# Optimization experiments

Hardware: AMD Instinct MI355X
Metric: run time of the kernel (lower is better)

## Reference

```python
import jax, jax.numpy as jnp
import numpy as np
from jax import lax

N_VAR, BATCH, N_IN, N_OUT, N_FEAT, T = 4, 32, 32, 32, 32, 256
EPS, COUPLING, GMAX, GMIN = 0.05, 0.2, 10.0, 0.01
DT, RMIN, RMAX, CMIN, CMAX = 0.1, 1e5, 1e7, 1e-7, 1e-4
ETA = np.array([0.05, 0.5, 0.3, 3.0], dtype=np.float32)  # printed-tanh activation params


def _init_theta(key, n_in, n_out):
    # xavier_uniform -> min-max normalize to [0,1], then bias-column construction as in pLayer.__init__
    a = float(np.sqrt(6.0 / (n_in + 2 + n_out)))
    t = jax.random.uniform(key, (n_in + 2, n_out), minval=-a, maxval=a)
    t = (t - t.min()) / (t.max() - t.min())
    t = t.at[-1, :].add(GMAX)
    t = t.at[-2, :].set(ETA[2] / (1.0 - ETA[2]) * (t[:-2].sum(0) + t[-1]))
    return t.astype(jnp.float32)


def setup_inputs():
    key = jax.random.key(0)
    kx, k1, k2 = jax.random.split(key, 3)
    x = jax.random.uniform(kx, (N_VAR, BATCH, N_IN, T), dtype=jnp.float32)
    theta1_ = _init_theta(k1, N_IN, N_OUT)
    theta2_ = _init_theta(k2, N_OUT * (N_FEAT + 1), N_OUT)
    # LearnableFilter init from beta_init (C_ fixed at -10, R_ is logit of normalized R)
    betas = np.linspace(0.1, 0.9, N_OUT)
    b0 = betas[:N_FEAT]
    b1 = betas[::-1][:N_FEAT]
    C_mean = 1.0 / (1.0 + np.exp(10.0)) * (CMAX - CMIN) + CMIN
    def r_(b):
        R_true = b * DT / (1.0 - b) / C_mean
        Rn = (R_true - RMIN) / (RMAX - RMIN)
        return np.log(Rn / (1.0 - Rn))
    Rlf_ = jnp.asarray(np.broadcast_to(np.stack([r_(b0), r_(b1)], -1), (N_OUT, N_FEAT, 2)).copy(), dtype=jnp.float32)
    Clf_ = jnp.full((N_OUT, N_FEAT, 2), -10.0, dtype=jnp.float32)
    return {"x": x, "theta1_": theta1_, "theta2_": theta2_, "Rlf_": Rlf_, "Clf_": Clf_}


def _theta_eff(theta_):
    # clamp + magnitude pruning with straight-through estimator
    t = jnp.clip(theta_, -GMAX, GMAX)
    t = jnp.where(jnp.abs(t) < GMIN, 0.0, t)
    return lax.stop_gradient(t) + theta_ - lax.stop_gradient(theta_)


def _pmac(a, theta_, key):
    # a: [N,B,Cin,T] -> [N,B,Cout,T]; printed MAC with sign-split weights and ideal inverter INV(a)=-a
    th = _theta_eff(theta_)
    noise = (jax.random.uniform(key, (N_VAR,) + th.shape) * 2.0 - 1.0) * EPS + 1.0
    thn = th[None] * noise  # [N,M,O]
    W = jnp.abs(thn) / (jnp.sum(jnp.abs(thn), axis=1, keepdims=True) + 1e-10)
    pos = (thn >= 0).astype(a.dtype)
    neg = 1.0 - pos
    ar = jnp.swapaxes(a, 2, 3)  # [N,B,T,Cin]
    ones = jnp.ones(ar.shape[:-1] + (1,), a.dtype)
    a_ext = jnp.concatenate([ar, ones, jnp.zeros_like(ones)], axis=-1)  # [N,B,T,M]
    a_neg = (-a_ext).at[..., -1].set(0.0)  # INV(a_ext) with last column zeroed
    z = jnp.einsum('nbtm,nmo->nbto', a_ext, W * pos) + jnp.einsum('nbtm,nmo->nbto', a_neg, W * neg)
    act = ETA[0] + ETA[1] * jnp.tanh((z - ETA[2]) * ETA[3])
    return jnp.swapaxes(act, 2, 3)


def _filter_bank(x, R_, C_, key):
    # x: [K,N,B,T]; first-order leaky integrator with fresh per-step R/C/mu noise, random init state
    K, N, B, Tt = x.shape
    Rt = jax.nn.sigmoid(R_) * (RMAX - RMIN) + RMIN  # [K]
    Ct = jax.nn.sigmoid(C_) * (CMAX - CMIN) + CMIN
    kR, kC, kmu, k0 = jax.random.split(key, 4)
    nR = (jax.random.uniform(kR, (Tt, K, N, 1)) * 2.0 - 1.0) * EPS + 1.0
    nC = (jax.random.uniform(kC, (Tt, K, N, 1)) * 2.0 - 1.0) * EPS + 1.0
    mu = jax.random.uniform(kmu, (Tt, K, N, 1)) * COUPLING + 1.0
    RC = mu * (Rt[None, :, None, None] * nR) * (Ct[None, :, None, None] * nC)
    beta = RC / (RC + DT)  # [T,K,N,1]
    s0 = jax.random.uniform(k0, (K, N, B))  # random_state=True
    xs = jnp.moveaxis(x, 3, 0)  # [T,K,N,B]
    def step(s, inp):
        x_t, b_t = inp
        return b_t * s + (1.0 - b_t) * x_t, s  # emit pre-update state (torch keeps init, drops last)
    _, outs = lax.scan(step, s0, (xs, beta))
    return jnp.moveaxis(outs, 0, 3)  # [K,N,B,T]


def reference(x, theta1_, theta2_, Rlf_, Clf_):
    key = jax.random.key(42)
    k1, k2, k3, k4 = jax.random.split(key, 4)
    a1 = _pmac(x, theta1_, k1)  # [N,B,C,T]
    N, B, C, Tt = a1.shape
    F = N_FEAT
    K = C * F
    xc = jnp.transpose(a1, (2, 0, 1, 3))  # [C,N,B,T]
    xk = jnp.broadcast_to(xc[:, None], (C, F, N, B, Tt)).reshape(K, N, B, Tt)
    y = _filter_bank(xk, Rlf_[..., 0].reshape(K), Clf_[..., 0].reshape(K), k2)
    y = _filter_bank(y, Rlf_[..., 1].reshape(K), Clf_[..., 1].reshape(K), k3)
    y = y.reshape(C, F, N, B, Tt)
    feats = jnp.concatenate([xc[:, None], y], axis=1)  # [C,F+1,N,B,T]
    h = jnp.transpose(feats, (2, 3, 0, 1, 4)).reshape(N, B, C * (F + 1), Tt)
    return _pmac(h, theta2_, k4)  # [N,B,N_out,T]
```

## Files before the change

### kernel.cpp

```cpp
#include <hip/hip_runtime.h>
#include <stdint.h>

#define C_RMIN 100000.0f
#define C_RMAX 10000000.0f
#define C_CMIN 1e-07f
#define C_CMAX 1e-04f
#define C_DT   0.1f
#define C_EPS  0.05f
#define C_COUP 0.2f

typedef __attribute__((ext_vector_type(8))) short bf16x8;
typedef __attribute__((ext_vector_type(4))) float floatx4;

__host__ __device__ inline void tf2x32(uint32_t k0, uint32_t k1,
                                       uint32_t& x0, uint32_t& x1) {
  uint32_t ks2 = k0 ^ k1 ^ 0x1BD11BDAu;
  uint32_t a = x0 + k0, b = x1 + k1;
#define TFR(r) a += b; b = (b << (r)) | (b >> (32 - (r))); b ^= a;
  TFR(13) TFR(15) TFR(26) TFR(6)
  a += k1;  b += ks2 + 1u;
  TFR(17) TFR(29) TFR(16) TFR(24)
  a += ks2; b += k0 + 2u;
  TFR(13) TFR(15) TFR(26) TFR(6)
  a += k0;  b += k1 + 3u;
  TFR(17) TFR(29) TFR(16) TFR(24)
  a += k1;  b += ks2 + 4u;
  TFR(13) TFR(15) TFR(26) TFR(6)
  a += ks2; b += k0 + 5u;
#undef TFR
  x0 = a; x1 = b;
}

__device__ inline float unif01(uint32_t k0, uint32_t k1, uint32_t e) {
  uint32_t x0 = 0u, x1 = e;
  tf2x32(k0, k1, x0, x1);
  uint32_t bits = x0 ^ x1;
  return __uint_as_float((bits >> 9) | 0x3F800000u) - 1.0f;
}

__device__ inline float theta_eff(float t) {
  t = fminf(fmaxf(t, -10.0f), 10.0f);
  return (fabsf(t) < 0.01f) ? 0.0f : t;
}

__device__ inline float sigmoidf(float x) { return 1.0f / (1.0f + expf(-x)); }

__device__ inline float noise_mul(float u) { return (u * 2.0f - 1.0f) * C_EPS + 1.0f; }

__global__ __launch_bounds__(256) void prep_kernel(
    const float* __restrict__ Rlf, const float* __restrict__ Clf,
    const float* __restrict__ theta1, const float* __restrict__ theta2,
    const float* __restrict__ x,
    float* __restrict__ beta12, float* __restrict__ a1,
    float* __restrict__ denom2p,
    uint32_t k1a, uint32_t k1b, uint32_t k4a, uint32_t k4b,
    uint32_t kR1a, uint32_t kR1b, uint32_t kC1a, uint32_t kC1b,
    uint32_t kM1a, uint32_t kM1b,
    uint32_t kR2a, uint32_t kR2b, uint32_t kC2a, uint32_t kC2b,
    uint32_t kM2a, uint32_t kM2b) {
  __shared__ float red[256];
  __shared__ float vsm[34 * 32];
  __shared__ float S1s[33 * 32];
  int bid = blockIdx.x;
  int tid = threadIdx.x;
  if (bid < 32) {
    int n = bid >> 3, p = bid & 7;
    int o = tid & 31;
    int jc = tid >> 5;
    int j0 = p * 8 + jc;
    float part = 0.0f;
    for (int j = j0; j < 1058; j += 64) {
      float t = theta_eff(theta2[j * 32 + o]);
      float u = unif01(k4a, k4b, (uint32_t)((n * 1058 + j) * 32 + o));
      part += fabsf(t * noise_mul(u));
    }
    red[jc * 32 + o] = part;
    __syncthreads();
    if (jc == 0) {
      float s = 0.0f;
      for (int q = 0; q < 8; ++q) s += red[q * 32 + o];
      denom2p[(n * 8 + p) * 32 + o] = s;
    }
  } else if (bid < 160) {
    int blk = bid - 32;
    int n = blk >> 5, b = blk & 31;
    int o = tid & 31, mq = tid >> 5;
    float dp = 0.0f;
    for (int m = mq; m < 34; m += 8) {
      float t = theta_eff(theta1[m * 32 + o]);
      float v = t * noise_mul(unif01(k1a, k1b, (uint32_t)((n * 34 + m) * 32 + o)));
      vsm[m * 32 + o] = v;
      dp += fabsf(v);
    }
    red[mq * 32 + o] = dp;
    __syncthreads();
    for (int idx = tid; idx < 33 * 32; idx += 256) {
      int oo = idx & 31;
      float den = 1e-10f;
#pragma unroll
      for (int q = 0; q < 8; ++q) den += red[q * 32 + oo];
      S1s[idx] = vsm[idx] / den;
    }
    __syncthreads();
    const float* xp = x + (size_t)((n * 32 + b) * 32) * 256;
    float acc[32];
#pragma unroll
    for (int oo = 0; oo < 32; ++oo) acc[oo] = S1s[32 * 32 + oo];
    for (int m = 0; m < 32; ++m) {
      float xm = xp[m * 256 + tid];
#pragma unroll
      for (int oo = 0; oo < 32; ++oo) acc[oo] += xm * S1s[m * 32 + oo];
    }
    float* ap = a1 + (size_t)((n * 32 + b) * 32) * 256;
#pragma unroll
    for (int oo = 0; oo < 32; ++oo)
      ap[oo * 256 + tid] = 0.05f + 0.5f * tanhf((acc[oo] - 0.3f) * 3.0f);
  } else {
    int u = (bid - 160) * 256 + tid;
    int k = u & 1023;
    int tc = (u >> 10) & 31;
    int n = u >> 15;
    float Rt1 = sigmoidf(Rlf[k * 2 + 0]) * (C_RMAX - C_RMIN) + C_RMIN;
    float Ct1 = sigmoidf(Clf[k * 2 + 0]) * (C_CMAX - C_CMIN) + C_CMIN;
    float Rt2 = sigmoidf(Rlf[k * 2 + 1]) * (C_RMAX - C_RMIN) + C_RMIN;
    float Ct2 = sigmoidf(Clf[k * 2 + 1]) * (C_CMAX - C_CMIN) + C_CMIN;
#pragma unroll
    for (int it = 0; it < 8; ++it) {
      int t = tc * 8 + it;
      uint32_t e = (uint32_t)((t * 1024 + k) * 4 + n);
      float nR1 = noise_mul(unif01(kR1a, kR1b, e));
      float nC1 = noise_mul(unif01(kC1a, kC1b, e));
      float mu1 = unif01(kM1a, kM1b, e) * C_COUP + 1.0f;
      float rc1 = mu1 * (Rt1 * nR1) * (Ct1 * nC1);
      float nR2 = noise_mul(unif01(kR2a, kR2b, e));
      float nC2 = noise_mul(unif01(kC2a, kC2b, e));
      float mu2 = unif01(kM2a, kM2b, e) * C_COUP + 1.0f;
      float rc2 = mu2 * (Rt2 * nR2) * (Ct2 * nC2);
      float2 bb = { rc1 / (rc1 + C_DT), rc2 / (rc2 + C_DT) };
      *(float2*)&beta12[(size_t)(((n * 256 + t) * 1024) + k) * 2] = bb;
    }
  }
}

#define YP 136
#define YPLANE (16 * YP)

__global__ __launch_bounds__(192) void fk8_kernel(
    const float* __restrict__ a1, const float* __restrict__ theta2,
    const float* __restrict__ denom2p,
    const float* __restrict__ beta12, float* __restrict__ zpart,
    uint32_t k01a, uint32_t k01b, uint32_t k02a, uint32_t k02b,
    uint32_t k4a, uint32_t k4b) {
  int bid = blockIdx.x;
  int g = bid & 31;
  int b = bid >> 5;
  int n = g >> 3, e = g & 7;
  int nb = n * 32 + b;
  int tid = threadIdx.x;

  __shared__ __align__(16) uint16_t yh[2 * YPLANE];
  __shared__ __align__(16) short wf[8 * 512];
  __shared__ float sden[32];

  const float* a1nb = a1 + (size_t)nb * 8192;
  const float* bp = beta12 + (size_t)n * 524288 + e * 256;
  float* zout = zpart + (size_t)bid * 8192;

  if (tid < 32) {
    float d = 1e-10f;
#pragma unroll
    for (int q = 0; q < 8; ++q) d += denom2p[(n * 8 + q) * 32 + tid];
    sden[tid] = d;
  }
  __syncthreads();

  float s1 = 0.0f, s2 = 0.0f;
  int cc = 0;

  for (int it = 0; it < 22; ++it) {
    int widx = it * 192 + tid;
    if (widx < 4096) {
      int j = widx & 7;
      int lane_ = (widx >> 3) & 63;
      int ot = (widx >> 9) & 1;
      int ks = widx >> 10;
      int sub = ((lane_ >> 4) << 3) + j;
      int jrow = (e * 4 + ks) * 33 + 1 + sub;
      int oo = ot * 16 + (lane_ & 15);
      float th = theta_eff(theta2[jrow * 32 + oo]);
      float u = unif01(k4a, k4b, (uint32_t)((n * 1058 + jrow) * 32 + oo));
      float w = th * noise_mul(u) / sden[oo];
      uint32_t wb = __float_as_uint(w);
      uint32_t hi = (wb + 0x7FFFu + ((wb >> 16) & 1u)) >> 16;
      wf[(ks * 2 + ot) * 512 + lane_ * 8 + j] = (short)(uint16_t)hi;
    }
  }
  if (tid < 128) {
    int k = e * 128 + tid;
    uint32_t e0 = (uint32_t)((k * 4 + n) * 32 + b);
    s1 = unif01(k01a, k01b, e0);
    s2 = unif01(k02a, k02b, e0);
    cc = k >> 5;
  }
  __syncthreads();

  for (int c = 0; c <= 16; ++c) {
    if (tid < 128) {
      if (c < 16) {
        uint16_t* yhb = yh + (c & 1) * YPLANE;
        int t0 = c * 16;
#pragma unroll
        for (int it = 0; it < 16; ++it) {
          int t = t0 + it;
          uint32_t sb = __float_as_uint(s2);
          uint32_t r = (sb + 0x7FFFu + ((sb >> 16) & 1u)) >> 16;
          yhb[it * YP + tid] = (uint16_t)r;
          float2 bb = *(const float2*)&bp[(size_t)t * 2048 + tid * 2];
          float xv = a1nb[cc * 256 + t];
          s2 = bb.y * (s2 - s1) + s1;
          s1 = bb.x * (s1 - xv) + xv;
        }
      }
    } else if (c >= 1) {
      int lane = tid - 128;
      int tc = lane & 15, q = lane >> 4;
      const uint16_t* yhr = yh + ((c - 1) & 1) * YPLANE + tc * YP + q * 8;
      floatx4 acc0a = {0,0,0,0}, acc0b = {0,0,0,0};
      floatx4 acc1a = {0,0,0,0}, acc1b = {0,0,0,0};
#pragma unroll
      for (int ks = 0; ks < 4; ++ks) {
        bf16x8 ah = *(const bf16x8*)(yhr + ks * 32);
        bf16x8 bh0 = *(const bf16x8*)&wf[(ks * 2 + 0) * 512 + lane * 8];
        bf16x8 bh1 = *(const bf16x8*)&wf[(ks * 2 + 1) * 512 + lane * 8];
        if (ks & 1) {
          acc0b = __builtin_amdgcn_mfma_f32_16x16x32_bf16(ah, bh0, acc0b, 0, 0, 0);
          acc1b = __builtin_amdgcn_mfma_f32_16x16x32_bf16(ah, bh1, acc1b, 0, 0, 0);
        } else {
          acc0a = __builtin_amdgcn_mfma_f32_16x16x32_bf16(ah, bh0, acc0a, 0, 0, 0);
          acc1a = __builtin_amdgcn_mfma_f32_16x16x32_bf16(ah, bh1, acc1a, 0, 0, 0);
        }
      }
      int t0 = (c - 1) * 16;
      floatx4 r0 = acc0a + acc0b;
      floatx4 r1 = acc1a + acc1b;
      *(floatx4*)&zout[tc * 256 + t0 + q * 4] = r0;
      *(floatx4*)&zout[(16 + tc) * 256 + t0 + q * 4] = r1;
    }
    __syncthreads();
  }
}

__global__ __launch_bounds__(256) void cb3_kernel(
    const float* __restrict__ a1, const float* __restrict__ theta2,
    const float* __restrict__ denom2p,
    const float* __restrict__ zpart, float* __restrict__ out,
    uint32_t k4a, uint32_t k4b) {
  int nb = blockIdx.x;
  int n = nb >> 5, b = nb & 31;
  int t = threadIdx.x;
  __shared__ float xs[32][256];
  __shared__ float wd[33 * 32];
  __shared__ float sden[32];
  if (t < 32) {
    float d = 1e-10f;
#pragma unroll
    for (int q = 0; q < 8; ++q) d += denom2p[(n * 8 + q) * 32 + t];
    sden[t] = d;
  }
  const float* a1nb = a1 + (size_t)nb * 8192;
  for (int c = 0; c < 32; ++c) xs[c][t] = a1nb[c * 256 + t];
  __syncthreads();
  for (int idx = t; idx < 33 * 32; idx += 256) {
    int r = idx >> 5, oo = idx & 31;
    int j = (r < 32) ? r * 33 : 1056;
    float th = theta_eff(theta2[j * 32 + oo]);
    float u = unif01(k4a, k4b, (uint32_t)((n * 1058 + j) * 32 + oo));
    wd[idx] = th * noise_mul(u) / sden[oo];
  }
  __syncthreads();
  const float* zp = zpart + (size_t)(b * 32 + n * 8) * 8192;
  float* op = out + (size_t)nb * 8192;
  for (int o = 0; o < 32; ++o) {
    float z = wd[32 * 32 + o];
#pragma unroll
    for (int c = 0; c < 32; ++c) z += xs[c][t] * wd[c * 32 + o];
#pragma unroll
    for (int e = 0; e < 8; ++e) z += zp[e * 8192 + o * 256 + t];
    op[o * 256 + t] = 0.05f + 0.5f * tanhf((z - 0.3f) * 3.0f);
  }
}

struct KeyPair { uint32_t a, b; };

static inline void split4_host(KeyPair key, KeyPair out[4]) {
  for (uint32_t i = 0; i < 4; ++i) {
    uint32_t x0 = 0u, x1 = i;
    tf2x32(key.a, key.b, x0, x1);
    out[i] = {x0, x1};
  }
}

extern "C" void kernel_launch(void* const* d_in, const int* in_sizes, int n_in,
                              void* d_out, int out_size, void* d_ws, size_t ws_size,
                              hipStream_t stream) {
  const float* x   = (const float*)d_in[0];
  const float* th1 = (const float*)d_in[1];
  const float* th2 = (const float*)d_in[2];
  const float* Rlf = (const float*)d_in[3];
  const float* Clf = (const float*)d_in[4];
  float* out = (float*)d_out;
  float* ws = (float*)d_ws;

  float* den2p  = ws;
  float* a1     = ws + 1024;
  float* beta12 = ws + 1049600;
  float* zpart  = ws + 3146752;

  KeyPair root{0u, 42u};
  KeyPair kk[4];  split4_host(root, kk);
  KeyPair f1[4];  split4_host(kk[1], f1);
  KeyPair f2[4];  split4_host(kk[2], f2);

  prep_kernel<<<dim3(672), dim3(256), 0, stream>>>(
      Rlf, Clf, th1, th2, x, beta12, a1, den2p,
      kk[0].a, kk[0].b, kk[3].a, kk[3].b,
      f1[0].a, f1[0].b, f1[1].a, f1[1].b, f1[2].a, f1[2].b,
      f2[0].a, f2[0].b, f2[1].a, f2[1].b, f2[2].a, f2[2].b);
  fk8_kernel<<<dim3(1024), dim3(192), 0, stream>>>(
      a1, th2, den2p, beta12, zpart,
      f1[3].a, f1[3].b, f2[3].a, f2[3].b, kk[3].a, kk[3].b);
  cb3_kernel<<<dim3(128), dim3(256), 0, stream>>>(
      a1, th2, den2p, zpart, out, kk[3].a, kk[3].b);
}
```

Measured before the change: 143.5 us.

## Prefetch next chunk of filter coefficients into registers and widen prep grid

The filter-scan threads now load the next 16 time steps of beta coefficients and inputs into registers while computing the current chunk. This hides global-load latency behind the serial recurrence. The prep kernel's beta generation is split into twice as many blocks with half the time steps each, for more parallelism. Launch bounds add a minimum-occupancy hint of 3 blocks per CU. The register double buffer raises register pressure and could spill.

```diff
diff --git a/kernel.cpp b/kernel.cpp
--- a/kernel.cpp
+++ b/kernel.cpp
@@ -118,15 +118,15 @@
   } else {
     int u = (bid - 160) * 256 + tid;
     int k = u & 1023;
-    int tc = (u >> 10) & 31;
-    int n = u >> 15;
+    int tc = (u >> 10) & 63;
+    int n = u >> 16;
     float Rt1 = sigmoidf(Rlf[k * 2 + 0]) * (C_RMAX - C_RMIN) + C_RMIN;
     float Ct1 = sigmoidf(Clf[k * 2 + 0]) * (C_CMAX - C_CMIN) + C_CMIN;
     float Rt2 = sigmoidf(Rlf[k * 2 + 1]) * (C_RMAX - C_RMIN) + C_RMIN;
     float Ct2 = sigmoidf(Clf[k * 2 + 1]) * (C_CMAX - C_CMIN) + C_CMIN;
 #pragma unroll
-    for (int it = 0; it < 8; ++it) {
-      int t = tc * 8 + it;
+    for (int it = 0; it < 4; ++it) {
+      int t = tc * 4 + it;
       uint32_t e = (uint32_t)((t * 1024 + k) * 4 + n);
       float nR1 = noise_mul(unif01(kR1a, kR1b, e));
       float nC1 = noise_mul(unif01(kC1a, kC1b, e));
@@ -145,7 +145,7 @@
 #define YP 136
 #define YPLANE (16 * YP)
 
-__global__ __launch_bounds__(192) void fk8_kernel(
+__global__ __launch_bounds__(192, 3) void fk9_kernel(
     const float* __restrict__ a1, const float* __restrict__ theta2,
     const float* __restrict__ denom2p,
     const float* __restrict__ beta12, float* __restrict__ zpart,
@@ -176,6 +176,8 @@
 
   float s1 = 0.0f, s2 = 0.0f;
   int cc = 0;
+  float2 breg[16];
+  float xreg[16];
 
   for (int it = 0; it < 22; ++it) {
     int widx = it * 192 + tid;
@@ -201,24 +203,41 @@
     s1 = unif01(k01a, k01b, e0);
     s2 = unif01(k02a, k02b, e0);
     cc = k >> 5;
+#pragma unroll
+    for (int it = 0; it < 16; ++it) {
+      breg[it] = *(const float2*)&bp[(size_t)it * 2048 + tid * 2];
+      xreg[it] = a1nb[cc * 256 + it];
+    }
   }
   __syncthreads();
 
   for (int c = 0; c <= 16; ++c) {
     if (tid < 128) {
       if (c < 16) {
+        float2 bnext[16];
+        float xnext[16];
+        if (c < 15) {
+#pragma unroll
+          for (int it = 0; it < 16; ++it) {
+            int t = (c + 1) * 16 + it;
+            bnext[it] = *(const float2*)&bp[(size_t)t * 2048 + tid * 2];
+            xnext[it] = a1nb[cc * 256 + t];
+          }
+        }
         uint16_t* yhb = yh + (c & 1) * YPLANE;
-        int t0 = c * 16;
 #pragma unroll
         for (int it = 0; it < 16; ++it) {
-          int t = t0 + it;
           uint32_t sb = __float_as_uint(s2);
           uint32_t r = (sb + 0x7FFFu + ((sb >> 16) & 1u)) >> 16;
           yhb[it * YP + tid] = (uint16_t)r;
-          float2 bb = *(const float2*)&bp[(size_t)t * 2048 + tid * 2];
-          float xv = a1nb[cc * 256 + t];
+          float2 bb = breg[it];
+          float xv = xreg[it];
           s2 = bb.y * (s2 - s1) + s1;
           s1 = bb.x * (s1 - xv) + xv;
+        }
+        if (c < 15) {
+#pragma unroll
+          for (int it = 0; it < 16; ++it) { breg[it] = bnext[it]; xreg[it] = xnext[it]; }
         }
       }
     } else if (c >= 1) {
@@ -321,12 +340,12 @@
   KeyPair f1[4];  split4_host(kk[1], f1);
   KeyPair f2[4];  split4_host(kk[2], f2);
 
-  prep_kernel<<<dim3(672), dim3(256), 0, stream>>>(
+  prep_kernel<<<dim3(1184), dim3(256), 0, stream>>>(
       Rlf, Clf, th1, th2, x, beta12, a1, den2p,
       kk[0].a, kk[0].b, kk[3].a, kk[3].b,
       f1[0].a, f1[0].b, f1[1].a, f1[1].b, f1[2].a, f1[2].b,
       f2[0].a, f2[0].b, f2[1].a, f2[1].b, f2[2].a, f2[2].b);
-  fk8_kernel<<<dim3(1024), dim3(192), 0, stream>>>(
+  fk9_kernel<<<dim3(1024), dim3(192), 0, stream>>>(
       a1, th2, den2p, beta12, zpart,
       f1[3].a, f1[3].b, f2[3].a, f2[3].b, kk[3].a, kk[3].b);
   cb3_kernel<<<dim3(128), dim3(256), 0, stream>>>(
```

Result: slower. 153.5 us (+7.0%).

## Precompute bf16 MFMA weight fragments once in prep kernel, defer denominator scaling

Applied to the files above, without the earlier changes.

The per-block weight fragment generation (theta clamp, threefry noise, bf16 rounding) in the filter kernel was repeated by every one of the 1024 blocks. It now happens once in 128 extra prep blocks that write to a global buffer, and each filter block copies its 8 KB slice into shared memory. The per-output denominator division is moved to the final combine kernel as a reciprocal multiply, because the prep stage cannot wait on the denominator reduction. This changes rounding slightly, since bf16 rounding now happens before normalization.

```diff
diff --git a/kernel.cpp b/kernel.cpp
--- a/kernel.cpp
+++ b/kernel.cpp
@@ -52,7 +52,7 @@
     const float* __restrict__ theta1, const float* __restrict__ theta2,
     const float* __restrict__ x,
     float* __restrict__ beta12, float* __restrict__ a1,
-    float* __restrict__ denom2p,
+    float* __restrict__ denom2p, uint16_t* __restrict__ wbuf,
     uint32_t k1a, uint32_t k1b, uint32_t k4a, uint32_t k4b,
     uint32_t kR1a, uint32_t kR1b, uint32_t kC1a, uint32_t kC1b,
     uint32_t kM1a, uint32_t kM1b,
@@ -115,7 +115,7 @@
 #pragma unroll
     for (int oo = 0; oo < 32; ++oo)
       ap[oo * 256 + tid] = 0.05f + 0.5f * tanhf((acc[oo] - 0.3f) * 3.0f);
-  } else {
+  } else if (bid < 672) {
     int u = (bid - 160) * 256 + tid;
     int k = u & 1023;
     int tc = (u >> 10) & 31;
@@ -139,18 +139,36 @@
       float2 bb = { rc1 / (rc1 + C_DT), rc2 / (rc2 + C_DT) };
       *(float2*)&beta12[(size_t)(((n * 256 + t) * 1024) + k) * 2] = bb;
     }
+  } else {
+#pragma unroll
+    for (int i = 0; i < 4; ++i) {
+      int widx = (bid - 672) * 1024 + i * 256 + tid;
+      int grp = widx >> 12;
+      int n = grp >> 3, e = grp & 7;
+      int w4 = widx & 4095;
+      int j = w4 & 7;
+      int lane_ = (w4 >> 3) & 63;
+      int ot = (w4 >> 9) & 1;
+      int ks = w4 >> 10;
+      int sub = ((lane_ >> 4) << 3) + j;
+      int jrow = (e * 4 + ks) * 33 + 1 + sub;
+      int oo = ot * 16 + (lane_ & 15);
+      float th = theta_eff(theta2[jrow * 32 + oo]);
+      float u = unif01(k4a, k4b, (uint32_t)((n * 1058 + jrow) * 32 + oo));
+      float w = th * noise_mul(u);
+      uint32_t wb = __float_as_uint(w);
+      wbuf[widx] = (uint16_t)((wb + 0x7FFFu + ((wb >> 16) & 1u)) >> 16);
+    }
   }
 }
 
 #define YP 136
 #define YPLANE (16 * YP)
 
-__global__ __launch_bounds__(192) void fk8_kernel(
-    const float* __restrict__ a1, const float* __restrict__ theta2,
-    const float* __restrict__ denom2p,
+__global__ __launch_bounds__(192) void fk10_kernel(
+    const float* __restrict__ a1, const uint16_t* __restrict__ wbuf,
     const float* __restrict__ beta12, float* __restrict__ zpart,
-    uint32_t k01a, uint32_t k01b, uint32_t k02a, uint32_t k02b,
-    uint32_t k4a, uint32_t k4b) {
+    uint32_t k01a, uint32_t k01b, uint32_t k02a, uint32_t k02b) {
   int bid = blockIdx.x;
   int g = bid & 31;
   int b = bid >> 5;
@@ -160,41 +178,19 @@
 
   __shared__ __align__(16) uint16_t yh[2 * YPLANE];
   __shared__ __align__(16) short wf[8 * 512];
-  __shared__ float sden[32];
 
   const float* a1nb = a1 + (size_t)nb * 8192;
   const float* bp = beta12 + (size_t)n * 524288 + e * 256;
   float* zout = zpart + (size_t)bid * 8192;
 
-  if (tid < 32) {
-    float d = 1e-10f;
-#pragma unroll
-    for (int q = 0; q < 8; ++q) d += denom2p[(n * 8 + q) * 32 + tid];
-    sden[tid] = d;
-  }
-  __syncthreads();
+  {
+    const uint4* wsrc = (const uint4*)(wbuf + (size_t)g * 4096);
+    uint4* wdst = (uint4*)wf;
+    for (int i = tid; i < 512; i += 192) wdst[i] = wsrc[i];
+  }
 
   float s1 = 0.0f, s2 = 0.0f;
   int cc = 0;
-
-  for (int it = 0; it < 22; ++it) {
-    int widx = it * 192 + tid;
-    if (widx < 4096) {
-      int j = widx & 7;
-      int lane_ = (widx >> 3) & 63;
-      int ot = (widx >> 9) & 1;
-      int ks = widx >> 10;
-      int sub = ((lane_ >> 4) << 3) + j;
-      int jrow = (e * 4 + ks) * 33 + 1 + sub;
-      int oo = ot * 16 + (lane_ & 15);
-      float th = theta_eff(theta2[jrow * 32 + oo]);
-      float u = unif01(k4a, k4b, (uint32_t)((n * 1058 + jrow) * 32 + oo));
-      float w = th * noise_mul(u) / sden[oo];
-      uint32_t wb = __float_as_uint(w);
-      uint32_t hi = (wb + 0x7FFFu + ((wb >> 16) & 1u)) >> 16;
-      wf[(ks * 2 + ot) * 512 + lane_ * 8 + j] = (short)(uint16_t)hi;
-    }
-  }
   if (tid < 128) {
     int k = e * 128 + tid;
     uint32_t e0 = (uint32_t)((k * 4 + n) * 32 + b);
@@ -250,7 +246,7 @@
   }
 }
 
-__global__ __launch_bounds__(256) void cb3_kernel(
+__global__ __launch_bounds__(256) void cb4_kernel(
     const float* __restrict__ a1, const float* __restrict__ theta2,
     const float* __restrict__ denom2p,
     const float* __restrict__ zpart, float* __restrict__ out,
@@ -261,11 +257,13 @@
   __shared__ float xs[32][256];
   __shared__ float wd[33 * 32];
   __shared__ float sden[32];
+  __shared__ float rsd[32];
   if (t < 32) {
     float d = 1e-10f;
 #pragma unroll
     for (int q = 0; q < 8; ++q) d += denom2p[(n * 8 + q) * 32 + t];
     sden[t] = d;
+    rsd[t] = 1.0f / d;
   }
   const float* a1nb = a1 + (size_t)nb * 8192;
   for (int c = 0; c < 32; ++c) xs[c][t] = a1nb[c * 256 + t];
@@ -284,8 +282,10 @@
     float z = wd[32 * 32 + o];
 #pragma unroll
     for (int c = 0; c < 32; ++c) z += xs[c][t] * wd[c * 32 + o];
-#pragma unroll
-    for (int e = 0; e < 8; ++e) z += zp[e * 8192 + o * 256 + t];
+    float zf = 0.0f;
+#pragma unroll
+    for (int e = 0; e < 8; ++e) zf += zp[e * 8192 + o * 256 + t];
+    z += zf * rsd[o];
     op[o * 256 + t] = 0.05f + 0.5f * tanhf((z - 0.3f) * 3.0f);
   }
 }
@@ -315,20 +315,21 @@
   float* a1     = ws + 1024;
   float* beta12 = ws + 1049600;
   float* zpart  = ws + 3146752;
+  uint16_t* wbuf = (uint16_t*)(ws + 11535360);
 
   KeyPair root{0u, 42u};
   KeyPair kk[4];  split4_host(root, kk);
   KeyPair f1[4];  split4_host(kk[1], f1);
   KeyPair f2[4];  split4_host(kk[2], f2);
 
-  prep_kernel<<<dim3(672), dim3(256), 0, stream>>>(
-      Rlf, Clf, th1, th2, x, beta12, a1, den2p,
+  prep_kernel<<<dim3(800), dim3(256), 0, stream>>>(
+      Rlf, Clf, th1, th2, x, beta12, a1, den2p, wbuf,
       kk[0].a, kk[0].b, kk[3].a, kk[3].b,
       f1[0].a, f1[0].b, f1[1].a, f1[1].b, f1[2].a, f1[2].b,
       f2[0].a, f2[0].b, f2[1].a, f2[1].b, f2[2].a, f2[2].b);
-  fk8_kernel<<<dim3(1024), dim3(192), 0, stream>>>(
-      a1, th2, den2p, beta12, zpart,
-      f1[3].a, f1[3].b, f2[3].a, f2[3].b, kk[3].a, kk[3].b);
-  cb3_kernel<<<dim3(128), dim3(256), 0, stream>>>(
+  fk10_kernel<<<dim3(1024), dim3(192), 0, stream>>>(
+      a1, wbuf, beta12, zpart,
+      f1[3].a, f1[3].b, f2[3].a, f2[3].b);
+  cb4_kernel<<<dim3(128), dim3(256), 0, stream>>>(
       a1, th2, den2p, zpart, out, kk[3].a, kk[3].b);
 }
```

Measured after the change: 134.9 us. 6.0% less time.
